# Optimization experiments

Measured on AMD Instinct MI355X. Metric: run time of the kernel, lower is better.

The kernel has to match this reference:

```python
import jax, jax.numpy as jnp
import numpy as np

N = 50000
E = 1600000
DIN = 100
D = 128
DOUT = 40
L = 3
EPS = 1e-5


def setup_inputs() -> dict:
    key = jax.random.key(0)
    ks = jax.random.split(key, 12)
    s = lambda *sh: 1.0 / np.sqrt(sh[-2] if len(sh) >= 2 else sh[-1])
    inp = {
        "x": jax.random.normal(ks[0], (N, DIN), jnp.float32),
        "edge_index": jax.random.randint(ks[1], (2, E), 0, N, jnp.int32),
        # node encoder (linear DIN -> D)
        "W_enc": jax.random.normal(ks[2], (DIN, D), jnp.float32) * (1.0 / np.sqrt(DIN)),
        "b_enc": jnp.zeros((D,), jnp.float32),
        # pre_mp linear D -> D
        "W_pre": jax.random.normal(ks[3], (D, D), jnp.float32) * (1.0 / np.sqrt(D)),
        "b_pre": jnp.zeros((D,), jnp.float32),
        # stacked GCN conv weights [L, D, D] and biases [L, D]
        "Wc": jax.random.normal(ks[4], (L, D, D), jnp.float32) * (1.0 / np.sqrt(D)),
        "bc": jnp.zeros((L, D), jnp.float32),
        # LayerNorm params for layers 0..L-2
        "ln_g": jnp.ones((L - 1, D), jnp.float32),
        "ln_b": jnp.zeros((L - 1, D), jnp.float32),
        # post_mp node head D -> DOUT
        "W_head": jax.random.normal(ks[5], (D, DOUT), jnp.float32) * (1.0 / np.sqrt(D)),
        "b_head": jnp.zeros((DOUT,), jnp.float32),
    }
    return inp


def _layer_norm(h, g, b):
    mu = jnp.mean(h, axis=-1, keepdims=True)
    var = jnp.mean(jnp.square(h - mu), axis=-1, keepdims=True)
    return (h - mu) * jax.lax.rsqrt(var + EPS) * g + b


def _gcn_forward(x, edge_index, W_enc, b_enc, W_pre, b_pre, Wc, bc, ln_g, ln_b, W_head, b_head):
    # feature encoder + pre-MP linear (dropout is identity in eval)
    h = x @ W_enc + b_enc
    h = h @ W_pre + b_pre

    # add self loops, compute symmetric GCN normalization once
    loop = jnp.arange(N, dtype=edge_index.dtype)
    src = jnp.concatenate([edge_index[0], loop])  # [E+N]
    dst = jnp.concatenate([edge_index[1], loop])
    deg = jax.ops.segment_sum(jnp.ones_like(dst, jnp.float32), dst, num_segments=N)
    dinv = jnp.where(deg > 0, jax.lax.rsqrt(jnp.maximum(deg, 1.0)), 0.0)
    norm = dinv[src] * dinv[dst]  # [E+N]

    for i in range(L):
        hw = h @ Wc[i]                              # [N, D] transform first
        msg = hw[src] * norm[:, None]               # gather + scale  [E+N, D]
        h = jax.ops.segment_sum(msg, dst, num_segments=N) + bc[i]
        if i < L - 1:
            h = _layer_norm(h, ln_g[i], ln_b[i])
            h = jax.nn.relu(h)
    # post-MP node classification head
    return h @ W_head + b_head


def reference(x, edge_index, W_enc, b_enc, W_pre, b_pre, Wc, bc, ln_g, ln_b, W_head, b_head):
    return _gcn_forward(x, edge_index, W_enc, b_enc, W_pre, b_pre, Wc, bc, ln_g, ln_b, W_head, b_head)
```

## Files before the change

kernel.cpp:

```cpp
#include <hip/hip_runtime.h>


#define NNODES 50000
#define NEDGES 1600000
#define DINN 100
#define DOUTN 40
#define CAP 96
#define NB1 ((NNODES + 255) / 256)
#define PDIV 687195u
#define NCHUNK 782
#define NGROUP 391
#define FE_GRID (NGROUP * 24)
#define MTILES ((NNODES + 63) / 64)

typedef __attribute__((ext_vector_type(8))) short short8;
typedef __attribute__((ext_vector_type(4))) float floatx4;

static __device__ __forceinline__ unsigned int f2bf(float f) {
    unsigned int u = __float_as_uint(f);
    return (u + 0x7fffu + ((u >> 16) & 1u)) >> 16;
}
static __device__ __forceinline__ float bflo(unsigned int u) { return __uint_as_float(u << 16); }
static __device__ __forceinline__ float bfhi(unsigned int u) { return __uint_as_float(u & 0xffff0000u); }

__global__ void init_ws(int* __restrict__ cursor, const float* __restrict__ Wpre,
                        const float* __restrict__ Wc, unsigned int* __restrict__ Wt) {
    int bid = blockIdx.x, tid = threadIdx.x;
    if (bid < NB1) {
        int n = bid * 256 + tid;
        if (n < NNODES) cursor[n] = 0;
    } else {
        int t = (bid - NB1) * 256 + tid;
        if (t < 4 * 8192) {
            int m = t >> 13, rem = t & 8191;
            int n = rem >> 6, k2 = rem & 63;
            const float* W = (m == 0) ? Wpre : (Wc + (size_t)(m - 1) * 16384);
            unsigned int lo = f2bf(W[(2 * k2) * 128 + n]);
            unsigned int hi = f2bf(W[(2 * k2 + 1) * 128 + n]);
            Wt[t] = lo | (hi << 16);
        }
    }
}

__global__ __launch_bounds__(256) void fill_enc(const int* __restrict__ src,
                                                const int* __restrict__ dst,
                                                int* __restrict__ cursor,
                                                unsigned short* __restrict__ colp,
                                                const float* __restrict__ x,
                                                const float* __restrict__ W_enc,
                                                const float* __restrict__ b_enc,
                                                unsigned int* __restrict__ C) {
    __shared__ float as[16][DINN];
    int bid = blockIdx.x, tid = threadIdx.x;
    int g = bid / 24, r = bid % 24;
    if (r < 16) {
        int p = bid & 7;
        int chunk = g * 2 + (r >> 3);
        int e0 = chunk * 2048;
#pragma unroll
        for (int k = 0; k < 8; k++) {
            int e = e0 + k * 256 + tid;
            if (e < NEDGES) {
                int d = dst[e];
                if ((int)(((unsigned long long)(unsigned)d * PDIV) >> 32) == p) {
                    int s = src[e];
                    int pos = atomicAdd(&cursor[d], 1);
                    if (pos < CAP) colp[(size_t)d * CAP + pos] = (unsigned short)s;
                }
            }
        }
    } else {
        int tile = g * 8 + (r - 16);
        int row0 = tile * 16;
        if (row0 >= NNODES) return;
        for (int idx = tid; idx < 16 * DINN; idx += 256) {
            int rr = idx / DINN, k = idx - rr * DINN;
            int row = row0 + rr;
            as[rr][k] = (row < NNODES) ? x[(size_t)row * DINN + k] : 0.0f;
        }
        __syncthreads();
        int c = tid & 63;
        int rg = tid >> 6;
        float acc0[4], acc1[4];
#pragma unroll
        for (int q = 0; q < 4; q++) { acc0[q] = 0.f; acc1[q] = 0.f; }
#pragma unroll 4
        for (int k = 0; k < DINN; k++) {
            float2 wv = *(const float2*)&W_enc[k * 128 + 2 * c];
#pragma unroll
            for (int q = 0; q < 4; q++) {
                float a = as[rg * 4 + q][k];
                acc0[q] += a * wv.x;
                acc1[q] += a * wv.y;
            }
        }
        float2 bb = *(const float2*)&b_enc[2 * c];
#pragma unroll
        for (int q = 0; q < 4; q++) {
            int row = row0 + rg * 4 + q;
            if (row < NNODES)
                C[(size_t)row * 64 + c] = f2bf(acc0[q] + bb.x) | (f2bf(acc1[q] + bb.y) << 16);
        }
    }
}

template <int MODE>
static __device__ __forceinline__ void mfma_body(unsigned char* smem, int bid,
                                                 const unsigned int* __restrict__ A,
                                                 const unsigned int* __restrict__ Bt,
                                                 const float* __restrict__ aux,
                                                 unsigned int* __restrict__ C, int M) {
    int tid = threadIdx.x;
    int row0 = bid * 64;
    for (int c = tid; c < 1024; c += 256) {
        int rr = c >> 4, c16 = c & 15;
        int grow = row0 + rr;
        uint4 p = (grow < M) ? *(const uint4*)&A[(size_t)grow * 64 + c16 * 4]
                             : make_uint4(0, 0, 0, 0);
        *(uint4*)&smem[(rr * 256 + c16 * 16) ^ ((rr & 7) << 4)] = p;
    }
    for (int c = tid; c < 2048; c += 256) {
        int n = c >> 4, k16 = c & 15;
        uint4 v = *(const uint4*)&Bt[n * 64 + k16 * 4];
        *(uint4*)&smem[16384 + ((n * 256 + k16 * 16) ^ ((n & 7) << 4))] = v;
    }
    __syncthreads();

    int lane = tid & 63, w = tid >> 6;
    int ml = lane & 15, kg = lane >> 4;
    short8 afrag[4];
#pragma unroll
    for (int k0 = 0; k0 < 4; k0++) {
        int rr = w * 16 + ml;
        uint4 t = *(uint4*)&smem[(rr * 256 + k0 * 64 + kg * 16) ^ ((rr & 7) << 4)];
        afrag[k0] = *(short8*)&t;
    }
#pragma unroll
    for (int n = 0; n < 8; n++) {
        floatx4 acc = {0.f, 0.f, 0.f, 0.f};
#pragma unroll
        for (int k0 = 0; k0 < 4; k0++) {
            int rn = n * 16 + ml;
            uint4 t = *(uint4*)&smem[16384 + ((rn * 256 + k0 * 64 + kg * 16) ^ ((rn & 7) << 4))];
            short8 b = *(short8*)&t;
            acc = __builtin_amdgcn_mfma_f32_16x16x32_bf16(afrag[k0], b, acc, 0, 0, 0);
        }
        int colc = n * 16 + ml;
        float bv = (MODE == 0) ? aux[colc] : 0.f;
#pragma unroll
        for (int q = 0; q < 4; q++) {
            int grow = row0 + w * 16 + kg * 4 + q;
            float v;
            if (MODE == 0) {
                v = acc[q] + bv;
            } else {
                float dv = (grow < M) ? aux[grow] : 0.f;
                v = acc[q] * dv;
            }
            float other = __shfl_xor(v, 1);
            if (!(lane & 1) && grow < M) {
                C[(size_t)grow * 64 + n * 8 + (ml >> 1)] = f2bf(v) | (f2bf(other) << 16);
            }
        }
    }
}

__global__ __launch_bounds__(256) void pre_mfma_dinv(const unsigned int* __restrict__ A,
                                                     const unsigned int* __restrict__ Bt,
                                                     const float* __restrict__ bias,
                                                     unsigned int* __restrict__ C,
                                                     const int* __restrict__ cursor,
                                                     float* __restrict__ dinv) {
    __shared__ __align__(16) unsigned char smem[49152];
    int bid = blockIdx.x;
    if (bid < MTILES) {
        mfma_body<0>(smem, bid, A, Bt, bias, C, NNODES);
    } else {
        int n = (bid - MTILES) * 256 + threadIdx.x;
        if (n < NNODES) dinv[n] = rsqrtf((float)(min(cursor[n], CAP) + 1));
    }
}

__global__ __launch_bounds__(256) void conv_mfma(const unsigned int* __restrict__ A,
                                                 const unsigned int* __restrict__ Bt,
                                                 const float* __restrict__ dinv,
                                                 unsigned int* __restrict__ C) {
    __shared__ __align__(16) unsigned char smem[49152];
    mfma_body<1>(smem, blockIdx.x, A, Bt, dinv, C, NNODES);
}

template <int LAST>
__global__ __launch_bounds__(256) void aggregate(const unsigned int* __restrict__ hw,
                                                 const unsigned short* __restrict__ colp,
                                                 const int* __restrict__ cursor,
                                                 const float* __restrict__ dinv,
                                                 const float* __restrict__ bias,
                                                 const float* __restrict__ g,
                                                 const float* __restrict__ b,
                                                 void* __restrict__ outv) {
    int row = blockIdx.x * 4 + (threadIdx.x >> 6);
    int lane = threadIdx.x & 63;
    if (row >= NNODES) return;
    int deg = min(cursor[row], CAP);
    const size_t cb = (size_t)row * CAP;
    unsigned int su = hw[(size_t)row * 64 + lane];
    float ax0 = bflo(su), ay0 = bfhi(su);
    float ax1 = 0.f, ay1 = 0.f, ax2 = 0.f, ay2 = 0.f, ax3 = 0.f, ay3 = 0.f;
    for (int j0 = 0; j0 < deg; j0 += 64) {
        int idx = j0 + lane;
        int myc = (idx < deg) ? (int)colp[cb + idx] : 0;
        int cnt = min(64, deg - j0);
        int j = 0;
        for (; j + 8 <= cnt; j += 8) {
            int s0 = __shfl(myc, j),     s1 = __shfl(myc, j + 1);
            int s2 = __shfl(myc, j + 2), s3 = __shfl(myc, j + 3);
            int s4 = __shfl(myc, j + 4), s5 = __shfl(myc, j + 5);
            int s6 = __shfl(myc, j + 6), s7 = __shfl(myc, j + 7);
            unsigned int u0 = hw[(size_t)s0 * 64 + lane];
            unsigned int u1 = hw[(size_t)s1 * 64 + lane];
            unsigned int u2 = hw[(size_t)s2 * 64 + lane];
            unsigned int u3 = hw[(size_t)s3 * 64 + lane];
            unsigned int u4 = hw[(size_t)s4 * 64 + lane];
            unsigned int u5 = hw[(size_t)s5 * 64 + lane];
            unsigned int u6 = hw[(size_t)s6 * 64 + lane];
            unsigned int u7 = hw[(size_t)s7 * 64 + lane];
            ax0 += bflo(u0); ay0 += bfhi(u0);
            ax1 += bflo(u1); ay1 += bfhi(u1);
            ax2 += bflo(u2); ay2 += bfhi(u2);
            ax3 += bflo(u3); ay3 += bfhi(u3);
            ax0 += bflo(u4); ay0 += bfhi(u4);
            ax1 += bflo(u5); ay1 += bfhi(u5);
            ax2 += bflo(u6); ay2 += bfhi(u6);
            ax3 += bflo(u7); ay3 += bfhi(u7);
        }
        for (; j < cnt; ++j) {
            int s = __shfl(myc, j);
            unsigned int u = hw[(size_t)s * 64 + lane];
            ax0 += bflo(u); ay0 += bfhi(u);
        }
    }
    float hx = ax0 + ax1 + ax2 + ax3;
    float hy = ay0 + ay1 + ay2 + ay3;
    float sc = dinv[row];
    float2 bb = *(const float2*)&bias[lane * 2];
    hx = hx * sc + bb.x;
    hy = hy * sc + bb.y;
    if (LAST == 0) {
        float sum = hx + hy;
#pragma unroll
        for (int off = 32; off >= 1; off >>= 1) sum += __shfl_xor(sum, off);
        float mu = sum * (1.0f / 128.0f);
        float dx = hx - mu, dy = hy - mu;
        float vs = dx * dx + dy * dy;
#pragma unroll
        for (int off = 32; off >= 1; off >>= 1) vs += __shfl_xor(vs, off);
        float rstd = rsqrtf(vs * (1.0f / 128.0f) + 1e-5f);
        float2 gg = *(const float2*)&g[lane * 2];
        float2 lb = *(const float2*)&b[lane * 2];
        hx = fmaxf(dx * rstd * gg.x + lb.x, 0.0f);
        hy = fmaxf(dy * rstd * gg.y + lb.y, 0.0f);
        ((unsigned int*)outv)[(size_t)row * 64 + lane] = f2bf(hx) | (f2bf(hy) << 16);
    } else {
        *(float2*)&((float*)outv)[(size_t)row * 128 + lane * 2] = make_float2(hx, hy);
    }
}

__global__ __launch_bounds__(256) void head_gemm(const float* __restrict__ h,
                                                 const float* __restrict__ W,
                                                 const float* __restrict__ bias,
                                                 float* __restrict__ out, int M) {
    __shared__ float hs[32][128];
    int tid = threadIdx.x;
    int row0 = blockIdx.x * 32;
    for (int idx = tid; idx < 32 * 128; idx += 256) {
        int rr = idx >> 7, k = idx & 127;
        int row = row0 + rr;
        hs[rr][k] = (row < M) ? h[(size_t)row * 128 + k] : 0.0f;
    }
    __syncthreads();
    int d = tid & 63;
    int rg = tid >> 6;
    if (d < DOUTN) {
        float acc[8];
#pragma unroll
        for (int q = 0; q < 8; q++) acc[q] = 0.0f;
#pragma unroll 4
        for (int k = 0; k < 128; k++) {
            float wv = W[k * DOUTN + d];
#pragma unroll
            for (int q = 0; q < 8; q++) acc[q] += hs[rg * 8 + q][k] * wv;
        }
        float bv = bias[d];
#pragma unroll
        for (int q = 0; q < 8; q++) {
            int row = row0 + rg * 8 + q;
            if (row < M) out[(size_t)row * DOUTN + d] = acc[q] + bv;
        }
    }
}

extern "C" void kernel_launch(void* const* d_in, const int* in_sizes, int n_in,
                              void* d_out, int out_size, void* d_ws, size_t ws_size,
                              hipStream_t stream) {
    const float* x = (const float*)d_in[0];
    const int* ei = (const int*)d_in[1];
    const int* esrc = ei;
    const int* edst = ei + NEDGES;
    const float* W_enc = (const float*)d_in[2];
    const float* b_enc = (const float*)d_in[3];
    const float* W_pre = (const float*)d_in[4];
    const float* b_pre = (const float*)d_in[5];
    const float* Wc = (const float*)d_in[6];
    const float* bc = (const float*)d_in[7];
    const float* ln_g = (const float*)d_in[8];
    const float* ln_b = (const float*)d_in[9];
    const float* W_head = (const float*)d_in[10];
    const float* b_head = (const float*)d_in[11];
    float* out = (float*)d_out;

    char* ws = (char*)d_ws;
    const size_t packBytes = (size_t)NNODES * 64 * 4;
    size_t off = 0;
    unsigned int* bufA = (unsigned int*)(ws + off); off += packBytes;
    unsigned int* bufB = (unsigned int*)(ws + off); off += packBytes;
    float* bufC = (float*)(ws + off); off += (size_t)NNODES * 128 * 4;
    float* dinv = (float*)(ws + off); off += (size_t)NNODES * 4;
    int* cursor = (int*)(ws + off); off += (size_t)NNODES * 4;
    unsigned int* Wt = (unsigned int*)(ws + off); off += (size_t)4 * 8192 * 4;
    unsigned short* colp = (unsigned short*)(ws + off); off += (size_t)NNODES * CAP * 2;

    init_ws<<<NB1 + 128, 256, 0, stream>>>(cursor, W_pre, Wc, Wt);

    fill_enc<<<FE_GRID, 256, 0, stream>>>(esrc, edst, cursor, colp, x, W_enc, b_enc, bufA);

    pre_mfma_dinv<<<MTILES + NB1, 256, 0, stream>>>(bufA, Wt, b_pre, bufB, cursor, dinv);

    for (int l = 0; l < 3; l++) {
        conv_mfma<<<MTILES, 256, 0, stream>>>(bufB, Wt + (size_t)(l + 1) * 8192, dinv, bufA);
        if (l < 2)
            aggregate<0><<<(NNODES + 3) / 4, 256, 0, stream>>>(
                bufA, colp, cursor, dinv, bc + (size_t)l * 128, ln_g + (size_t)l * 128,
                ln_b + (size_t)l * 128, bufB);
        else
            aggregate<1><<<(NNODES + 3) / 4, 256, 0, stream>>>(
                bufA, colp, cursor, dinv, bc + (size_t)l * 128, nullptr, nullptr, bufC);
    }

    head_gemm<<<(NNODES + 31) / 32, 256, 0, stream>>>(bufC, W_head, b_head, out, NNODES);
}
```

Baseline: 354.4 us.

## Fuse head GEMM into last aggregate and process two rows per wavefront

The aggregation kernel now handles two destination rows per wavefront and interleaves their neighbor gathers, so more independent loads are in flight. The final layer's aggregate computes the 128->40 head projection directly from registers with shuffles and a shared-memory copy of W_head. This removes the head_gemm kernel and the fp32 intermediate buffer round-trip. The dinv computation also drops the CAP clamp on degree, which changes the normalization when a node has more than CAP in-edges, and the shuffle-based head loop is serial per row.

```diff
diff --git a/kernel.cpp b/kernel.cpp
--- a/kernel.cpp
+++ b/kernel.cpp
@@ -8,7 +8,6 @@
 #define CAP 96
 #define NB1 ((NNODES + 255) / 256)
 #define PDIV 687195u
-#define NCHUNK 782
 #define NGROUP 391
 #define FE_GRID (NGROUP * 24)
 #define MTILES ((NNODES + 63) / 64)
@@ -177,7 +176,7 @@
         mfma_body<0>(smem, bid, A, Bt, bias, C, NNODES);
     } else {
         int n = (bid - MTILES) * 256 + threadIdx.x;
-        if (n < NNODES) dinv[n] = rsqrtf((float)(min(cursor[n], CAP) + 1));
+        if (n < NNODES) dinv[n] = rsqrtf((float)(cursor[n] + 1));
     }
 }
 
@@ -197,104 +196,122 @@
                                                  const float* __restrict__ bias,
                                                  const float* __restrict__ g,
                                                  const float* __restrict__ b,
-                                                 void* __restrict__ outv) {
-    int row = blockIdx.x * 4 + (threadIdx.x >> 6);
-    int lane = threadIdx.x & 63;
-    if (row >= NNODES) return;
-    int deg = min(cursor[row], CAP);
-    const size_t cb = (size_t)row * CAP;
-    unsigned int su = hw[(size_t)row * 64 + lane];
-    float ax0 = bflo(su), ay0 = bfhi(su);
-    float ax1 = 0.f, ay1 = 0.f, ax2 = 0.f, ay2 = 0.f, ax3 = 0.f, ay3 = 0.f;
-    for (int j0 = 0; j0 < deg; j0 += 64) {
-        int idx = j0 + lane;
-        int myc = (idx < deg) ? (int)colp[cb + idx] : 0;
-        int cnt = min(64, deg - j0);
-        int j = 0;
-        for (; j + 8 <= cnt; j += 8) {
-            int s0 = __shfl(myc, j),     s1 = __shfl(myc, j + 1);
-            int s2 = __shfl(myc, j + 2), s3 = __shfl(myc, j + 3);
-            int s4 = __shfl(myc, j + 4), s5 = __shfl(myc, j + 5);
-            int s6 = __shfl(myc, j + 6), s7 = __shfl(myc, j + 7);
-            unsigned int u0 = hw[(size_t)s0 * 64 + lane];
-            unsigned int u1 = hw[(size_t)s1 * 64 + lane];
-            unsigned int u2 = hw[(size_t)s2 * 64 + lane];
-            unsigned int u3 = hw[(size_t)s3 * 64 + lane];
-            unsigned int u4 = hw[(size_t)s4 * 64 + lane];
-            unsigned int u5 = hw[(size_t)s5 * 64 + lane];
-            unsigned int u6 = hw[(size_t)s6 * 64 + lane];
-            unsigned int u7 = hw[(size_t)s7 * 64 + lane];
-            ax0 += bflo(u0); ay0 += bfhi(u0);
-            ax1 += bflo(u1); ay1 += bfhi(u1);
-            ax2 += bflo(u2); ay2 += bfhi(u2);
-            ax3 += bflo(u3); ay3 += bfhi(u3);
-            ax0 += bflo(u4); ay0 += bfhi(u4);
-            ax1 += bflo(u5); ay1 += bfhi(u5);
-            ax2 += bflo(u6); ay2 += bfhi(u6);
-            ax3 += bflo(u7); ay3 += bfhi(u7);
-        }
-        for (; j < cnt; ++j) {
-            int s = __shfl(myc, j);
-            unsigned int u = hw[(size_t)s * 64 + lane];
+                                                 void* __restrict__ outv,
+                                                 const float* __restrict__ Wh,
+                                                 const float* __restrict__ bh) {
+    __shared__ float whs[LAST ? 128 * DOUTN : 1];
+    int tid = threadIdx.x, lane = tid & 63;
+    if (LAST) {
+        for (int i = tid; i < 128 * DOUTN; i += 256) whs[i] = Wh[i];
+        __syncthreads();
+    }
+    int wid = blockIdx.x * 4 + (tid >> 6);
+    int r0 = wid * 2;
+    if (r0 >= NNODES) return;
+    int r1 = r0 + 1;
+    int deg0 = min(cursor[r0], CAP), deg1 = min(cursor[r1], CAP);
+    const unsigned short* cp0 = &colp[(size_t)r0 * CAP];
+    const unsigned short* cp1 = &colp[(size_t)r1 * CAP];
+    int c0 = min(deg0, 64), c1 = min(deg1, 64);
+    int myc0 = (lane < c0) ? (int)cp0[lane] : 0;
+    int myc1 = (lane < c1) ? (int)cp1[lane] : 0;
+    float ax0 = 0.f, ay0 = 0.f, px0 = 0.f, py0 = 0.f;
+    float ax1 = 0.f, ay1 = 0.f, px1 = 0.f, py1 = 0.f;
+    int m = min(c0, c1) & ~7;
+    int j = 0;
+    for (; j < m; j += 8) {
+        int s0 = __shfl(myc0, j),     s1 = __shfl(myc0, j + 1);
+        int s2 = __shfl(myc0, j + 2), s3 = __shfl(myc0, j + 3);
+        int s4 = __shfl(myc0, j + 4), s5 = __shfl(myc0, j + 5);
+        int s6 = __shfl(myc0, j + 6), s7 = __shfl(myc0, j + 7);
+        int t0 = __shfl(myc1, j),     t1 = __shfl(myc1, j + 1);
+        int t2 = __shfl(myc1, j + 2), t3 = __shfl(myc1, j + 3);
+        int t4 = __shfl(myc1, j + 4), t5 = __shfl(myc1, j + 5);
+        int t6 = __shfl(myc1, j + 6), t7 = __shfl(myc1, j + 7);
+        unsigned u0 = hw[(size_t)s0 * 64 + lane], u1 = hw[(size_t)s1 * 64 + lane];
+        unsigned u2 = hw[(size_t)s2 * 64 + lane], u3 = hw[(size_t)s3 * 64 + lane];
+        unsigned u4 = hw[(size_t)s4 * 64 + lane], u5 = hw[(size_t)s5 * 64 + lane];
+        unsigned u6 = hw[(size_t)s6 * 64 + lane], u7 = hw[(size_t)s7 * 64 + lane];
+        unsigned v0 = hw[(size_t)t0 * 64 + lane], v1 = hw[(size_t)t1 * 64 + lane];
+        unsigned v2 = hw[(size_t)t2 * 64 + lane], v3 = hw[(size_t)t3 * 64 + lane];
+        unsigned v4 = hw[(size_t)t4 * 64 + lane], v5 = hw[(size_t)t5 * 64 + lane];
+        unsigned v6 = hw[(size_t)t6 * 64 + lane], v7 = hw[(size_t)t7 * 64 + lane];
+        ax0 += bflo(u0) + bflo(u1); ay0 += bfhi(u0) + bfhi(u1);
+        px0 += bflo(u2) + bflo(u3); py0 += bfhi(u2) + bfhi(u3);
+        ax0 += bflo(u4) + bflo(u5); ay0 += bfhi(u4) + bfhi(u5);
+        px0 += bflo(u6) + bflo(u7); py0 += bfhi(u6) + bfhi(u7);
+        ax1 += bflo(v0) + bflo(v1); ay1 += bfhi(v0) + bfhi(v1);
+        px1 += bflo(v2) + bflo(v3); py1 += bfhi(v2) + bfhi(v3);
+        ax1 += bflo(v4) + bflo(v5); ay1 += bfhi(v4) + bfhi(v5);
+        px1 += bflo(v6) + bflo(v7); py1 += bfhi(v6) + bfhi(v7);
+    }
+    for (; j < c0; ++j) {
+        int s = __shfl(myc0, j);
+        unsigned u = hw[(size_t)s * 64 + lane];
+        ax0 += bflo(u); ay0 += bfhi(u);
+    }
+    for (j = m; j < c1; ++j) {
+        int s = __shfl(myc1, j);
+        unsigned u = hw[(size_t)s * 64 + lane];
+        ax1 += bflo(u); ay1 += bfhi(u);
+    }
+    for (int j0 = 64; j0 < deg0; j0 += 64) {
+        int cc = min(64, deg0 - j0);
+        int mc = (lane < cc) ? (int)cp0[j0 + lane] : 0;
+        for (int k = 0; k < cc; ++k) {
+            int s = __shfl(mc, k);
+            unsigned u = hw[(size_t)s * 64 + lane];
             ax0 += bflo(u); ay0 += bfhi(u);
         }
     }
-    float hx = ax0 + ax1 + ax2 + ax3;
-    float hy = ay0 + ay1 + ay2 + ay3;
-    float sc = dinv[row];
-    float2 bb = *(const float2*)&bias[lane * 2];
-    hx = hx * sc + bb.x;
-    hy = hy * sc + bb.y;
-    if (LAST == 0) {
-        float sum = hx + hy;
-#pragma unroll
-        for (int off = 32; off >= 1; off >>= 1) sum += __shfl_xor(sum, off);
-        float mu = sum * (1.0f / 128.0f);
-        float dx = hx - mu, dy = hy - mu;
-        float vs = dx * dx + dy * dy;
-#pragma unroll
-        for (int off = 32; off >= 1; off >>= 1) vs += __shfl_xor(vs, off);
-        float rstd = rsqrtf(vs * (1.0f / 128.0f) + 1e-5f);
-        float2 gg = *(const float2*)&g[lane * 2];
-        float2 lb = *(const float2*)&b[lane * 2];
-        hx = fmaxf(dx * rstd * gg.x + lb.x, 0.0f);
-        hy = fmaxf(dy * rstd * gg.y + lb.y, 0.0f);
-        ((unsigned int*)outv)[(size_t)row * 64 + lane] = f2bf(hx) | (f2bf(hy) << 16);
-    } else {
-        *(float2*)&((float*)outv)[(size_t)row * 128 + lane * 2] = make_float2(hx, hy);
-    }
-}
-
-__global__ __launch_bounds__(256) void head_gemm(const float* __restrict__ h,
-                                                 const float* __restrict__ W,
-                                                 const float* __restrict__ bias,
-                                                 float* __restrict__ out, int M) {
-    __shared__ float hs[32][128];
-    int tid = threadIdx.x;
-    int row0 = blockIdx.x * 32;
-    for (int idx = tid; idx < 32 * 128; idx += 256) {
-        int rr = idx >> 7, k = idx & 127;
-        int row = row0 + rr;
-        hs[rr][k] = (row < M) ? h[(size_t)row * 128 + k] : 0.0f;
-    }
-    __syncthreads();
-    int d = tid & 63;
-    int rg = tid >> 6;
-    if (d < DOUTN) {
-        float acc[8];
-#pragma unroll
-        for (int q = 0; q < 8; q++) acc[q] = 0.0f;
+    for (int j0 = 64; j0 < deg1; j0 += 64) {
+        int cc = min(64, deg1 - j0);
+        int mc = (lane < cc) ? (int)cp1[j0 + lane] : 0;
+        for (int k = 0; k < cc; ++k) {
+            int s = __shfl(mc, k);
+            unsigned u = hw[(size_t)s * 64 + lane];
+            ax1 += bflo(u); ay1 += bfhi(u);
+        }
+    }
+
+    float hxa[2] = {ax0 + px0, ax1 + px1};
+    float hya[2] = {ay0 + py0, ay1 + py1};
+#pragma unroll
+    for (int q = 0; q < 2; q++) {
+        int row = r0 + q;
+        unsigned su = hw[(size_t)row * 64 + lane];
+        float hx = hxa[q] + bflo(su);
+        float hy = hya[q] + bfhi(su);
+        float sc = dinv[row];
+        float2 bb = *(const float2*)&bias[lane * 2];
+        hx = hx * sc + bb.x;
+        hy = hy * sc + bb.y;
+        if (LAST == 0) {
+            float sum = hx + hy;
+#pragma unroll
+            for (int off = 32; off >= 1; off >>= 1) sum += __shfl_xor(sum, off);
+            float mu = sum * (1.0f / 128.0f);
+            float dx = hx - mu, dy = hy - mu;
+            float vs = dx * dx + dy * dy;
+#pragma unroll
+            for (int off = 32; off >= 1; off >>= 1) vs += __shfl_xor(vs, off);
+            float rstd = rsqrtf(vs * (1.0f / 128.0f) + 1e-5f);
+            float2 gg = *(const float2*)&g[lane * 2];
+            float2 lb = *(const float2*)&b[lane * 2];
+            hx = fmaxf(dx * rstd * gg.x + lb.x, 0.0f);
+            hy = fmaxf(dy * rstd * gg.y + lb.y, 0.0f);
+            ((unsigned int*)outv)[(size_t)row * 64 + lane] = f2bf(hx) | (f2bf(hy) << 16);
+        } else {
+            float acc = (lane < DOUTN) ? bh[lane] : 0.f;
 #pragma unroll 4
-        for (int k = 0; k < 128; k++) {
-            float wv = W[k * DOUTN + d];
-#pragma unroll
-            for (int q = 0; q < 8; q++) acc[q] += hs[rg * 8 + q][k] * wv;
-        }
-        float bv = bias[d];
-#pragma unroll
-        for (int q = 0; q < 8; q++) {
-            int row = row0 + rg * 8 + q;
-            if (row < M) out[(size_t)row * DOUTN + d] = acc[q] + bv;
+            for (int k = 0; k < 64; k++) {
+                float hxk = __shfl(hx, k);
+                float hyk = __shfl(hy, k);
+                if (lane < DOUTN)
+                    acc += hxk * whs[(2 * k) * DOUTN + lane] +
+                           hyk * whs[(2 * k + 1) * DOUTN + lane];
+            }
+            if (lane < DOUTN) ((float*)outv)[(size_t)row * DOUTN + lane] = acc;
         }
     }
 }
@@ -323,7 +340,6 @@
     size_t off = 0;
     unsigned int* bufA = (unsigned int*)(ws + off); off += packBytes;
     unsigned int* bufB = (unsigned int*)(ws + off); off += packBytes;
-    float* bufC = (float*)(ws + off); off += (size_t)NNODES * 128 * 4;
     float* dinv = (float*)(ws + off); off += (size_t)NNODES * 4;
     int* cursor = (int*)(ws + off); off += (size_t)NNODES * 4;
     unsigned int* Wt = (unsigned int*)(ws + off); off += (size_t)4 * 8192 * 4;
@@ -338,13 +354,12 @@
     for (int l = 0; l < 3; l++) {
         conv_mfma<<<MTILES, 256, 0, stream>>>(bufB, Wt + (size_t)(l + 1) * 8192, dinv, bufA);
         if (l < 2)
-            aggregate<0><<<(NNODES + 3) / 4, 256, 0, stream>>>(
+            aggregate<0><<<(NNODES / 8), 256, 0, stream>>>(
                 bufA, colp, cursor, dinv, bc + (size_t)l * 128, ln_g + (size_t)l * 128,
-                ln_b + (size_t)l * 128, bufB);
+                ln_b + (size_t)l * 128, bufB, nullptr, nullptr);
         else
-            aggregate<1><<<(NNODES + 3) / 4, 256, 0, stream>>>(
-                bufA, colp, cursor, dinv, bc + (size_t)l * 128, nullptr, nullptr, bufC);
-    }
-
-    head_gemm<<<(NNODES + 31) / 32, 256, 0, stream>>>(bufC, W_head, b_head, out, NNODES);
-}
+            aggregate<1><<<(NNODES / 8), 256, 0, stream>>>(
+                bufA, colp, cursor, dinv, bc + (size_t)l * 128, nullptr, nullptr, out,
+                W_head, b_head);
+    }
+}
```

Result: slower. 419.0 us (+18.2%).

## Split GCN aggregation into two feature-half passes for cache-resident gathers

Applied to the files above, without the earlier changes.

The conv GEMM now writes its output as two separate 64-column bf16 halves. Aggregation runs as two kernels, one per half, so each gather table is 6.4 MB instead of 12.8 MB and is more likely to stay in cache; each wavefront processes two edges at once with half-width rows. The first half's fp32 result is staged in a scratch buffer, and the second kernel reads it back to apply LayerNorm. This costs an extra launch and extra scratch traffic. The dinv computation also changes to use the uncapped degree.

```diff
diff --git a/kernel.cpp b/kernel.cpp
--- a/kernel.cpp
+++ b/kernel.cpp
@@ -8,7 +8,6 @@
 #define CAP 96
 #define NB1 ((NNODES + 255) / 256)
 #define PDIV 687195u
-#define NCHUNK 782
 #define NGROUP 391
 #define FE_GRID (NGROUP * 24)
 #define MTILES ((NNODES + 63) / 64)
@@ -109,7 +108,8 @@
                                                  const unsigned int* __restrict__ A,
                                                  const unsigned int* __restrict__ Bt,
                                                  const float* __restrict__ aux,
-                                                 unsigned int* __restrict__ C, int M) {
+                                                 unsigned int* __restrict__ C,
+                                                 unsigned int* __restrict__ CB, int M) {
     int tid = threadIdx.x;
     int row0 = bid * 64;
     for (int c = tid; c < 1024; c += 256) {
@@ -159,7 +159,15 @@
             }
             float other = __shfl_xor(v, 1);
             if (!(lane & 1) && grow < M) {
-                C[(size_t)grow * 64 + n * 8 + (ml >> 1)] = f2bf(v) | (f2bf(other) << 16);
+                unsigned int pk = f2bf(v) | (f2bf(other) << 16);
+                if (MODE == 0) {
+                    C[(size_t)grow * 64 + n * 8 + (ml >> 1)] = pk;
+                } else {
+                    if (n < 4)
+                        C[(size_t)grow * 32 + n * 8 + (ml >> 1)] = pk;
+                    else
+                        CB[(size_t)grow * 32 + (n - 4) * 8 + (ml >> 1)] = pk;
+                }
             }
         }
     }
@@ -174,94 +182,128 @@
     __shared__ __align__(16) unsigned char smem[49152];
     int bid = blockIdx.x;
     if (bid < MTILES) {
-        mfma_body<0>(smem, bid, A, Bt, bias, C, NNODES);
+        mfma_body<0>(smem, bid, A, Bt, bias, C, nullptr, NNODES);
     } else {
         int n = (bid - MTILES) * 256 + threadIdx.x;
-        if (n < NNODES) dinv[n] = rsqrtf((float)(min(cursor[n], CAP) + 1));
+        if (n < NNODES) dinv[n] = rsqrtf((float)(cursor[n] + 1));
     }
 }
 
 __global__ __launch_bounds__(256) void conv_mfma(const unsigned int* __restrict__ A,
                                                  const unsigned int* __restrict__ Bt,
                                                  const float* __restrict__ dinv,
-                                                 unsigned int* __restrict__ C) {
+                                                 unsigned int* __restrict__ CA,
+                                                 unsigned int* __restrict__ CB) {
     __shared__ __align__(16) unsigned char smem[49152];
-    mfma_body<1>(smem, blockIdx.x, A, Bt, dinv, C, NNODES);
-}
-
-template <int LAST>
-__global__ __launch_bounds__(256) void aggregate(const unsigned int* __restrict__ hw,
-                                                 const unsigned short* __restrict__ colp,
-                                                 const int* __restrict__ cursor,
-                                                 const float* __restrict__ dinv,
-                                                 const float* __restrict__ bias,
-                                                 const float* __restrict__ g,
-                                                 const float* __restrict__ b,
-                                                 void* __restrict__ outv) {
-    int row = blockIdx.x * 4 + (threadIdx.x >> 6);
-    int lane = threadIdx.x & 63;
+    mfma_body<1>(smem, blockIdx.x, A, Bt, dinv, CA, CB, NNODES);
+}
+
+template <int H, int LAST>
+__global__ __launch_bounds__(256) void aggregate_half(const unsigned int* __restrict__ hw,
+                                                      const unsigned short* __restrict__ colp,
+                                                      const int* __restrict__ cursor,
+                                                      const float* __restrict__ dinv,
+                                                      const float* __restrict__ bias,
+                                                      const float* __restrict__ g,
+                                                      const float* __restrict__ b,
+                                                      float* __restrict__ sA,
+                                                      void* __restrict__ outv) {
+    int tid = threadIdx.x, lane = tid & 63;
+    int row = blockIdx.x * 4 + (tid >> 6);
     if (row >= NNODES) return;
+    int lh = lane & 31;
+    int hi = lane >> 5;
     int deg = min(cursor[row], CAP);
-    const size_t cb = (size_t)row * CAP;
-    unsigned int su = hw[(size_t)row * 64 + lane];
-    float ax0 = bflo(su), ay0 = bfhi(su);
-    float ax1 = 0.f, ay1 = 0.f, ax2 = 0.f, ay2 = 0.f, ax3 = 0.f, ay3 = 0.f;
-    for (int j0 = 0; j0 < deg; j0 += 64) {
-        int idx = j0 + lane;
-        int myc = (idx < deg) ? (int)colp[cb + idx] : 0;
-        int cnt = min(64, deg - j0);
-        int j = 0;
-        for (; j + 8 <= cnt; j += 8) {
-            int s0 = __shfl(myc, j),     s1 = __shfl(myc, j + 1);
-            int s2 = __shfl(myc, j + 2), s3 = __shfl(myc, j + 3);
-            int s4 = __shfl(myc, j + 4), s5 = __shfl(myc, j + 5);
-            int s6 = __shfl(myc, j + 6), s7 = __shfl(myc, j + 7);
-            unsigned int u0 = hw[(size_t)s0 * 64 + lane];
-            unsigned int u1 = hw[(size_t)s1 * 64 + lane];
-            unsigned int u2 = hw[(size_t)s2 * 64 + lane];
-            unsigned int u3 = hw[(size_t)s3 * 64 + lane];
-            unsigned int u4 = hw[(size_t)s4 * 64 + lane];
-            unsigned int u5 = hw[(size_t)s5 * 64 + lane];
-            unsigned int u6 = hw[(size_t)s6 * 64 + lane];
-            unsigned int u7 = hw[(size_t)s7 * 64 + lane];
-            ax0 += bflo(u0); ay0 += bfhi(u0);
-            ax1 += bflo(u1); ay1 += bfhi(u1);
-            ax2 += bflo(u2); ay2 += bfhi(u2);
-            ax3 += bflo(u3); ay3 += bfhi(u3);
-            ax0 += bflo(u4); ay0 += bfhi(u4);
-            ax1 += bflo(u5); ay1 += bfhi(u5);
-            ax2 += bflo(u6); ay2 += bfhi(u6);
-            ax3 += bflo(u7); ay3 += bfhi(u7);
-        }
-        for (; j < cnt; ++j) {
-            int s = __shfl(myc, j);
-            unsigned int u = hw[(size_t)s * 64 + lane];
-            ax0 += bflo(u); ay0 += bfhi(u);
-        }
-    }
-    float hx = ax0 + ax1 + ax2 + ax3;
-    float hy = ay0 + ay1 + ay2 + ay3;
+    const unsigned short* cp = &colp[(size_t)row * CAP];
+    int cnt = min(deg, 64);
+    int myc = (lane < cnt) ? (int)cp[lane] : 0;
+    float ax = 0.f, ay = 0.f, px = 0.f, py = 0.f;
+    int j0 = 0;
+    for (; j0 + 16 <= cnt; j0 += 16) {
+        int e = j0 + hi;
+        int s0 = __shfl(myc, e),      s1 = __shfl(myc, e + 2);
+        int s2 = __shfl(myc, e + 4),  s3 = __shfl(myc, e + 6);
+        int s4 = __shfl(myc, e + 8),  s5 = __shfl(myc, e + 10);
+        int s6 = __shfl(myc, e + 12), s7 = __shfl(myc, e + 14);
+        unsigned u0 = hw[(size_t)s0 * 32 + lh], u1 = hw[(size_t)s1 * 32 + lh];
+        unsigned u2 = hw[(size_t)s2 * 32 + lh], u3 = hw[(size_t)s3 * 32 + lh];
+        unsigned u4 = hw[(size_t)s4 * 32 + lh], u5 = hw[(size_t)s5 * 32 + lh];
+        unsigned u6 = hw[(size_t)s6 * 32 + lh], u7 = hw[(size_t)s7 * 32 + lh];
+        ax += bflo(u0) + bflo(u1); ay += bfhi(u0) + bfhi(u1);
+        px += bflo(u2) + bflo(u3); py += bfhi(u2) + bfhi(u3);
+        ax += bflo(u4) + bflo(u5); ay += bfhi(u4) + bfhi(u5);
+        px += bflo(u6) + bflo(u7); py += bfhi(u6) + bfhi(u7);
+    }
+    if (j0 < cnt) {
+        int e = j0 + hi;
+        int cm = cnt - 1;
+        int s0 = __shfl(myc, min(e, cm)),      s1 = __shfl(myc, min(e + 2, cm));
+        int s2 = __shfl(myc, min(e + 4, cm)),  s3 = __shfl(myc, min(e + 6, cm));
+        int s4 = __shfl(myc, min(e + 8, cm)),  s5 = __shfl(myc, min(e + 10, cm));
+        int s6 = __shfl(myc, min(e + 12, cm)), s7 = __shfl(myc, min(e + 14, cm));
+        unsigned u0 = (e < cnt) ? hw[(size_t)s0 * 32 + lh] : 0u;
+        unsigned u1 = (e + 2 < cnt) ? hw[(size_t)s1 * 32 + lh] : 0u;
+        unsigned u2 = (e + 4 < cnt) ? hw[(size_t)s2 * 32 + lh] : 0u;
+        unsigned u3 = (e + 6 < cnt) ? hw[(size_t)s3 * 32 + lh] : 0u;
+        unsigned u4 = (e + 8 < cnt) ? hw[(size_t)s4 * 32 + lh] : 0u;
+        unsigned u5 = (e + 10 < cnt) ? hw[(size_t)s5 * 32 + lh] : 0u;
+        unsigned u6 = (e + 12 < cnt) ? hw[(size_t)s6 * 32 + lh] : 0u;
+        unsigned u7 = (e + 14 < cnt) ? hw[(size_t)s7 * 32 + lh] : 0u;
+        ax += bflo(u0) + bflo(u1); ay += bfhi(u0) + bfhi(u1);
+        px += bflo(u2) + bflo(u3); py += bfhi(u2) + bfhi(u3);
+        ax += bflo(u4) + bflo(u5); ay += bfhi(u4) + bfhi(u5);
+        px += bflo(u6) + bflo(u7); py += bfhi(u6) + bfhi(u7);
+    }
+    for (int base = 64; base < deg; base += 64) {
+        int cc = min(64, deg - base);
+        int mc = (lane < cc) ? (int)cp[base + lane] : 0;
+        for (int j = 0; j < cc; j += 2) {
+            int e = j + hi;
+            int s = __shfl(mc, min(e, cc - 1));
+            unsigned u = (e < cc) ? hw[(size_t)s * 32 + lh] : 0u;
+            ax += bflo(u); ay += bfhi(u);
+        }
+    }
+    ax += px; ay += py;
+    ax += __shfl_xor(ax, 32);
+    ay += __shfl_xor(ay, 32);
+    unsigned su = hw[(size_t)row * 32 + lh];
     float sc = dinv[row];
-    float2 bb = *(const float2*)&bias[lane * 2];
-    hx = hx * sc + bb.x;
-    hy = hy * sc + bb.y;
-    if (LAST == 0) {
-        float sum = hx + hy;
-#pragma unroll
-        for (int off = 32; off >= 1; off >>= 1) sum += __shfl_xor(sum, off);
-        float mu = sum * (1.0f / 128.0f);
-        float dx = hx - mu, dy = hy - mu;
-        float vs = dx * dx + dy * dy;
-#pragma unroll
-        for (int off = 32; off >= 1; off >>= 1) vs += __shfl_xor(vs, off);
-        float rstd = rsqrtf(vs * (1.0f / 128.0f) + 1e-5f);
-        float2 gg = *(const float2*)&g[lane * 2];
-        float2 lb = *(const float2*)&b[lane * 2];
-        hx = fmaxf(dx * rstd * gg.x + lb.x, 0.0f);
-        hy = fmaxf(dy * rstd * gg.y + lb.y, 0.0f);
-        ((unsigned int*)outv)[(size_t)row * 64 + lane] = f2bf(hx) | (f2bf(hy) << 16);
+    float2 bb = *(const float2*)&bias[(H ? 64 : 0) + 2 * lh];
+    float hx = (ax + bflo(su)) * sc + bb.x;
+    float hy = (ay + bfhi(su)) * sc + bb.y;
+    if (H == 0) {
+        if (LAST == 0) {
+            if (hi == 0) *(float2*)&sA[(size_t)row * 64 + 2 * lh] = make_float2(hx, hy);
+        } else {
+            if (hi == 0)
+                *(float2*)&((float*)outv)[(size_t)row * 128 + 2 * lh] = make_float2(hx, hy);
+        }
     } else {
-        *(float2*)&((float*)outv)[(size_t)row * 128 + lane * 2] = make_float2(hx, hy);
+        if (LAST == 1) {
+            if (hi == 1)
+                *(float2*)&((float*)outv)[(size_t)row * 128 + 64 + 2 * lh] =
+                    make_float2(hx, hy);
+        } else {
+            float2 av = *(const float2*)&sA[(size_t)row * 64 + 2 * lh];
+            float sum = av.x + av.y + hx + hy;
+#pragma unroll
+            for (int off = 16; off >= 1; off >>= 1) sum += __shfl_xor(sum, off);
+            float mu = sum * (1.0f / 128.0f);
+            float dA0 = av.x - mu, dA1 = av.y - mu;
+            float dB0 = hx - mu, dB1 = hy - mu;
+            float vs = dA0 * dA0 + dA1 * dA1 + dB0 * dB0 + dB1 * dB1;
+#pragma unroll
+            for (int off = 16; off >= 1; off >>= 1) vs += __shfl_xor(vs, off);
+            float rstd = rsqrtf(vs * (1.0f / 128.0f) + 1e-5f);
+            float v0 = hi ? dB0 : dA0;
+            float v1 = hi ? dB1 : dA1;
+            float2 gg = *(const float2*)&g[2 * lane];
+            float2 lb = *(const float2*)&b[2 * lane];
+            float o0 = fmaxf(v0 * rstd * gg.x + lb.x, 0.0f);
+            float o1 = fmaxf(v1 * rstd * gg.y + lb.y, 0.0f);
+            ((unsigned int*)outv)[(size_t)row * 64 + lane] = f2bf(o0) | (f2bf(o1) << 16);
+        }
     }
 }
 
@@ -319,10 +361,12 @@
     float* out = (float*)d_out;
 
     char* ws = (char*)d_ws;
-    const size_t packBytes = (size_t)NNODES * 64 * 4;
     size_t off = 0;
-    unsigned int* bufA = (unsigned int*)(ws + off); off += packBytes;
-    unsigned int* bufB = (unsigned int*)(ws + off); off += packBytes;
+    unsigned int* F1 = (unsigned int*)(ws + off); off += (size_t)NNODES * 64 * 4;
+    unsigned int* F2 = (unsigned int*)(ws + off); off += (size_t)NNODES * 64 * 4;
+    unsigned int* hwA = (unsigned int*)(ws + off); off += (size_t)NNODES * 32 * 4;
+    unsigned int* hwB = (unsigned int*)(ws + off); off += (size_t)NNODES * 32 * 4;
+    float* sA = (float*)(ws + off); off += (size_t)NNODES * 64 * 4;
     float* bufC = (float*)(ws + off); off += (size_t)NNODES * 128 * 4;
     float* dinv = (float*)(ws + off); off += (size_t)NNODES * 4;
     int* cursor = (int*)(ws + off); off += (size_t)NNODES * 4;
@@ -331,19 +375,25 @@
 
     init_ws<<<NB1 + 128, 256, 0, stream>>>(cursor, W_pre, Wc, Wt);
 
-    fill_enc<<<FE_GRID, 256, 0, stream>>>(esrc, edst, cursor, colp, x, W_enc, b_enc, bufA);
-
-    pre_mfma_dinv<<<MTILES + NB1, 256, 0, stream>>>(bufA, Wt, b_pre, bufB, cursor, dinv);
-
+    fill_enc<<<FE_GRID, 256, 0, stream>>>(esrc, edst, cursor, colp, x, W_enc, b_enc, F1);
+
+    pre_mfma_dinv<<<MTILES + NB1, 256, 0, stream>>>(F1, Wt, b_pre, F2, cursor, dinv);
+
+    const int AGG_GRID = (NNODES + 3) / 4;
     for (int l = 0; l < 3; l++) {
-        conv_mfma<<<MTILES, 256, 0, stream>>>(bufB, Wt + (size_t)(l + 1) * 8192, dinv, bufA);
-        if (l < 2)
-            aggregate<0><<<(NNODES + 3) / 4, 256, 0, stream>>>(
-                bufA, colp, cursor, dinv, bc + (size_t)l * 128, ln_g + (size_t)l * 128,
-                ln_b + (size_t)l * 128, bufB);
-        else
-            aggregate<1><<<(NNODES + 3) / 4, 256, 0, stream>>>(
-                bufA, colp, cursor, dinv, bc + (size_t)l * 128, nullptr, nullptr, bufC);
+        conv_mfma<<<MTILES, 256, 0, stream>>>(F2, Wt + (size_t)(l + 1) * 8192, dinv, hwA, hwB);
+        if (l < 2) {
+            aggregate_half<0, 0><<<AGG_GRID, 256, 0, stream>>>(
+                hwA, colp, cursor, dinv, bc + (size_t)l * 128, nullptr, nullptr, sA, F2);
+            aggregate_half<1, 0><<<AGG_GRID, 256, 0, stream>>>(
+                hwB, colp, cursor, dinv, bc + (size_t)l * 128, ln_g + (size_t)l * 128,
+                ln_b + (size_t)l * 128, sA, F2);
+        } else {
+            aggregate_half<0, 1><<<AGG_GRID, 256, 0, stream>>>(
+                hwA, colp, cursor, dinv, bc + (size_t)l * 128, nullptr, nullptr, sA, bufC);
+            aggregate_half<1, 1><<<AGG_GRID, 256, 0, stream>>>(
+                hwB, colp, cursor, dinv, bc + (size_t)l * 128, nullptr, nullptr, sA, bufC);
+        }
     }
 
     head_gemm<<<(NNODES + 31) / 32, 256, 0, stream>>>(bufC, W_head, b_head, out, NNODES);
```

After: 364.2 us. 1.03x slower.

## Fold pre-MP linear into first conv weight and compute dinv inline

Applied to the files above, without the earlier changes.

Precomputes W_pre·Wc[0] and b_pre·Wc[0] in the init kernel, so the separate pre-MP GEMM pass over all nodes is removed and the first conv GEMM adds the folded bias before degree scaling. The dinv array is dropped; both the conv GEMM epilogue and the aggregation recompute rsqrt(deg+1) from the cursor counts. The final aggregation now writes bf16 packed features instead of fp32, which halves the traffic into the head GEMM. The trade-offs are bf16 rounding of the fused weight product and final activations. The normalisation now uses the uncapped degree, which differs from the earlier capped value whenever a node exceeds CAP.

```diff
diff --git a/kernel.cpp b/kernel.cpp
--- a/kernel.cpp
+++ b/kernel.cpp
@@ -8,7 +8,6 @@
 #define CAP 96
 #define NB1 ((NNODES + 255) / 256)
 #define PDIV 687195u
-#define NCHUNK 782
 #define NGROUP 391
 #define FE_GRID (NGROUP * 24)
 #define MTILES ((NNODES + 63) / 64)
@@ -24,20 +23,40 @@
 static __device__ __forceinline__ float bfhi(unsigned int u) { return __uint_as_float(u & 0xffff0000u); }
 
 __global__ void init_ws(int* __restrict__ cursor, const float* __restrict__ Wpre,
-                        const float* __restrict__ Wc, unsigned int* __restrict__ Wt) {
+                        const float* __restrict__ Wc, const float* __restrict__ b_pre,
+                        unsigned int* __restrict__ Wt, float* __restrict__ v0) {
     int bid = blockIdx.x, tid = threadIdx.x;
     if (bid < NB1) {
         int n = bid * 256 + tid;
         if (n < NNODES) cursor[n] = 0;
+    } else if (bid < NB1 + 64) {
+        int tt = (bid - NB1) * 256 + tid;
+        int mm = 2 + (tt >> 13);
+        int rem = tt & 8191;
+        int n = rem >> 6, k2 = rem & 63;
+        const float* W = Wc + (size_t)(mm - 1) * 16384;
+        unsigned int lo = f2bf(W[(2 * k2) * 128 + n]);
+        unsigned int hi = f2bf(W[(2 * k2 + 1) * 128 + n]);
+        Wt[mm * 8192 + n * 64 + k2] = lo | (hi << 16);
+    } else if (bid < NB1 + 96) {
+        int t = (bid - NB1 - 64) * 256 + tid;
+        int n = t >> 6, k2 = t & 63;
+        const float* wp0 = Wpre + (size_t)(2 * k2) * 128;
+        const float* wp1 = wp0 + 128;
+        float d0 = 0.f, d1 = 0.f;
+#pragma unroll 4
+        for (int j = 0; j < 128; j++) {
+            float wc = Wc[j * 128 + n];
+            d0 += wp0[j] * wc;
+            d1 += wp1[j] * wc;
+        }
+        Wt[8192 + n * 64 + k2] = f2bf(d0) | (f2bf(d1) << 16);
     } else {
-        int t = (bid - NB1) * 256 + tid;
-        if (t < 4 * 8192) {
-            int m = t >> 13, rem = t & 8191;
-            int n = rem >> 6, k2 = rem & 63;
-            const float* W = (m == 0) ? Wpre : (Wc + (size_t)(m - 1) * 16384);
-            unsigned int lo = f2bf(W[(2 * k2) * 128 + n]);
-            unsigned int hi = f2bf(W[(2 * k2 + 1) * 128 + n]);
-            Wt[t] = lo | (hi << 16);
+        if (tid < 128) {
+            float d = 0.f;
+#pragma unroll 4
+            for (int j = 0; j < 128; j++) d += b_pre[j] * Wc[j * 128 + tid];
+            v0[tid] = d;
         }
     }
 }
@@ -104,14 +123,16 @@
     }
 }
 
-template <int MODE>
-static __device__ __forceinline__ void mfma_body(unsigned char* smem, int bid,
-                                                 const unsigned int* __restrict__ A,
+template <int BIASV>
+__global__ __launch_bounds__(256) void conv_mfma(const unsigned int* __restrict__ A,
                                                  const unsigned int* __restrict__ Bt,
-                                                 const float* __restrict__ aux,
-                                                 unsigned int* __restrict__ C, int M) {
+                                                 const int* __restrict__ cursor,
+                                                 const float* __restrict__ v0,
+                                                 unsigned int* __restrict__ C) {
+    __shared__ __align__(16) unsigned char smem[49152];
     int tid = threadIdx.x;
-    int row0 = bid * 64;
+    int row0 = blockIdx.x * 64;
+    const int M = NNODES;
     for (int c = tid; c < 1024; c += 256) {
         int rr = c >> 4, c16 = c & 15;
         int grow = row0 + rr;
@@ -135,6 +156,12 @@
         uint4 t = *(uint4*)&smem[(rr * 256 + k0 * 64 + kg * 16) ^ ((rr & 7) << 4)];
         afrag[k0] = *(short8*)&t;
     }
+    float dvq[4];
+#pragma unroll
+    for (int q = 0; q < 4; q++) {
+        int grow = row0 + w * 16 + kg * 4 + q;
+        dvq[q] = (grow < M) ? rsqrtf((float)(cursor[grow] + 1)) : 0.f;
+    }
 #pragma unroll
     for (int n = 0; n < 8; n++) {
         floatx4 acc = {0.f, 0.f, 0.f, 0.f};
@@ -146,17 +173,11 @@
             acc = __builtin_amdgcn_mfma_f32_16x16x32_bf16(afrag[k0], b, acc, 0, 0, 0);
         }
         int colc = n * 16 + ml;
-        float bv = (MODE == 0) ? aux[colc] : 0.f;
+        float bv = BIASV ? v0[colc] : 0.f;
 #pragma unroll
         for (int q = 0; q < 4; q++) {
             int grow = row0 + w * 16 + kg * 4 + q;
-            float v;
-            if (MODE == 0) {
-                v = acc[q] + bv;
-            } else {
-                float dv = (grow < M) ? aux[grow] : 0.f;
-                v = acc[q] * dv;
-            }
+            float v = (acc[q] + bv) * dvq[q];
             float other = __shfl_xor(v, 1);
             if (!(lane & 1) && grow < M) {
                 C[(size_t)grow * 64 + n * 8 + (ml >> 1)] = f2bf(v) | (f2bf(other) << 16);
@@ -165,50 +186,26 @@
     }
 }
 
-__global__ __launch_bounds__(256) void pre_mfma_dinv(const unsigned int* __restrict__ A,
-                                                     const unsigned int* __restrict__ Bt,
-                                                     const float* __restrict__ bias,
-                                                     unsigned int* __restrict__ C,
-                                                     const int* __restrict__ cursor,
-                                                     float* __restrict__ dinv) {
-    __shared__ __align__(16) unsigned char smem[49152];
-    int bid = blockIdx.x;
-    if (bid < MTILES) {
-        mfma_body<0>(smem, bid, A, Bt, bias, C, NNODES);
-    } else {
-        int n = (bid - MTILES) * 256 + threadIdx.x;
-        if (n < NNODES) dinv[n] = rsqrtf((float)(min(cursor[n], CAP) + 1));
-    }
-}
-
-__global__ __launch_bounds__(256) void conv_mfma(const unsigned int* __restrict__ A,
-                                                 const unsigned int* __restrict__ Bt,
-                                                 const float* __restrict__ dinv,
-                                                 unsigned int* __restrict__ C) {
-    __shared__ __align__(16) unsigned char smem[49152];
-    mfma_body<1>(smem, blockIdx.x, A, Bt, dinv, C, NNODES);
-}
-
 template <int LAST>
 __global__ __launch_bounds__(256) void aggregate(const unsigned int* __restrict__ hw,
                                                  const unsigned short* __restrict__ colp,
                                                  const int* __restrict__ cursor,
-                                                 const float* __restrict__ dinv,
                                                  const float* __restrict__ bias,
                                                  const float* __restrict__ g,
                                                  const float* __restrict__ b,
-                                                 void* __restrict__ outv) {
+                                                 unsigned int* __restrict__ outp) {
     int row = blockIdx.x * 4 + (threadIdx.x >> 6);
     int lane = threadIdx.x & 63;
     if (row >= NNODES) return;
-    int deg = min(cursor[row], CAP);
-    const size_t cb = (size_t)row * CAP;
+    int curs = cursor[row];
+    int deg = min(curs, CAP);
+    const unsigned short* cp = &colp[(size_t)row * CAP];
     unsigned int su = hw[(size_t)row * 64 + lane];
     float ax0 = bflo(su), ay0 = bfhi(su);
     float ax1 = 0.f, ay1 = 0.f, ax2 = 0.f, ay2 = 0.f, ax3 = 0.f, ay3 = 0.f;
     for (int j0 = 0; j0 < deg; j0 += 64) {
         int idx = j0 + lane;
-        int myc = (idx < deg) ? (int)colp[cb + idx] : 0;
+        int myc = (idx < deg) ? (int)cp[idx] : 0;
         int cnt = min(64, deg - j0);
         int j = 0;
         for (; j + 8 <= cnt; j += 8) {
@@ -216,14 +213,14 @@
             int s2 = __shfl(myc, j + 2), s3 = __shfl(myc, j + 3);
             int s4 = __shfl(myc, j + 4), s5 = __shfl(myc, j + 5);
             int s6 = __shfl(myc, j + 6), s7 = __shfl(myc, j + 7);
-            unsigned int u0 = hw[(size_t)s0 * 64 + lane];
-            unsigned int u1 = hw[(size_t)s1 * 64 + lane];
-            unsigned int u2 = hw[(size_t)s2 * 64 + lane];
-            unsigned int u3 = hw[(size_t)s3 * 64 + lane];
-            unsigned int u4 = hw[(size_t)s4 * 64 + lane];
-            unsigned int u5 = hw[(size_t)s5 * 64 + lane];
-            unsigned int u6 = hw[(size_t)s6 * 64 + lane];
-            unsigned int u7 = hw[(size_t)s7 * 64 + lane];
+            unsigned u0 = hw[(size_t)s0 * 64 + lane];
+            unsigned u1 = hw[(size_t)s1 * 64 + lane];
+            unsigned u2 = hw[(size_t)s2 * 64 + lane];
+            unsigned u3 = hw[(size_t)s3 * 64 + lane];
+            unsigned u4 = hw[(size_t)s4 * 64 + lane];
+            unsigned u5 = hw[(size_t)s5 * 64 + lane];
+            unsigned u6 = hw[(size_t)s6 * 64 + lane];
+            unsigned u7 = hw[(size_t)s7 * 64 + lane];
             ax0 += bflo(u0); ay0 += bfhi(u0);
             ax1 += bflo(u1); ay1 += bfhi(u1);
             ax2 += bflo(u2); ay2 += bfhi(u2);
@@ -235,13 +232,13 @@
         }
         for (; j < cnt; ++j) {
             int s = __shfl(myc, j);
-            unsigned int u = hw[(size_t)s * 64 + lane];
+            unsigned u = hw[(size_t)s * 64 + lane];
             ax0 += bflo(u); ay0 += bfhi(u);
         }
     }
     float hx = ax0 + ax1 + ax2 + ax3;
     float hy = ay0 + ay1 + ay2 + ay3;
-    float sc = dinv[row];
+    float sc = rsqrtf((float)(curs + 1));
     float2 bb = *(const float2*)&bias[lane * 2];
     hx = hx * sc + bb.x;
     hy = hy * sc + bb.y;
@@ -259,23 +256,23 @@
         float2 lb = *(const float2*)&b[lane * 2];
         hx = fmaxf(dx * rstd * gg.x + lb.x, 0.0f);
         hy = fmaxf(dy * rstd * gg.y + lb.y, 0.0f);
-        ((unsigned int*)outv)[(size_t)row * 64 + lane] = f2bf(hx) | (f2bf(hy) << 16);
-    } else {
-        *(float2*)&((float*)outv)[(size_t)row * 128 + lane * 2] = make_float2(hx, hy);
-    }
-}
-
-__global__ __launch_bounds__(256) void head_gemm(const float* __restrict__ h,
+    }
+    outp[(size_t)row * 64 + lane] = f2bf(hx) | (f2bf(hy) << 16);
+}
+
+__global__ __launch_bounds__(256) void head_gemm(const unsigned int* __restrict__ h,
                                                  const float* __restrict__ W,
                                                  const float* __restrict__ bias,
                                                  float* __restrict__ out, int M) {
     __shared__ float hs[32][128];
     int tid = threadIdx.x;
     int row0 = blockIdx.x * 32;
-    for (int idx = tid; idx < 32 * 128; idx += 256) {
-        int rr = idx >> 7, k = idx & 127;
+    for (int idx = tid; idx < 32 * 64; idx += 256) {
+        int rr = idx >> 6, c = idx & 63;
         int row = row0 + rr;
-        hs[rr][k] = (row < M) ? h[(size_t)row * 128 + k] : 0.0f;
+        unsigned u = (row < M) ? h[(size_t)row * 64 + c] : 0u;
+        hs[rr][2 * c] = bflo(u);
+        hs[rr][2 * c + 1] = bfhi(u);
     }
     __syncthreads();
     int d = tid & 63;
@@ -321,30 +318,28 @@
     char* ws = (char*)d_ws;
     const size_t packBytes = (size_t)NNODES * 64 * 4;
     size_t off = 0;
-    unsigned int* bufA = (unsigned int*)(ws + off); off += packBytes;
-    unsigned int* bufB = (unsigned int*)(ws + off); off += packBytes;
-    float* bufC = (float*)(ws + off); off += (size_t)NNODES * 128 * 4;
-    float* dinv = (float*)(ws + off); off += (size_t)NNODES * 4;
+    unsigned int* F1 = (unsigned int*)(ws + off); off += packBytes;
+    unsigned int* F2 = (unsigned int*)(ws + off); off += packBytes;
+    unsigned int* hw = (unsigned int*)(ws + off); off += packBytes;
     int* cursor = (int*)(ws + off); off += (size_t)NNODES * 4;
     unsigned int* Wt = (unsigned int*)(ws + off); off += (size_t)4 * 8192 * 4;
+    float* v0 = (float*)(ws + off); off += 512;
     unsigned short* colp = (unsigned short*)(ws + off); off += (size_t)NNODES * CAP * 2;
 
-    init_ws<<<NB1 + 128, 256, 0, stream>>>(cursor, W_pre, Wc, Wt);
-
-    fill_enc<<<FE_GRID, 256, 0, stream>>>(esrc, edst, cursor, colp, x, W_enc, b_enc, bufA);
-
-    pre_mfma_dinv<<<MTILES + NB1, 256, 0, stream>>>(bufA, Wt, b_pre, bufB, cursor, dinv);
-
-    for (int l = 0; l < 3; l++) {
-        conv_mfma<<<MTILES, 256, 0, stream>>>(bufB, Wt + (size_t)(l + 1) * 8192, dinv, bufA);
-        if (l < 2)
-            aggregate<0><<<(NNODES + 3) / 4, 256, 0, stream>>>(
-                bufA, colp, cursor, dinv, bc + (size_t)l * 128, ln_g + (size_t)l * 128,
-                ln_b + (size_t)l * 128, bufB);
-        else
-            aggregate<1><<<(NNODES + 3) / 4, 256, 0, stream>>>(
-                bufA, colp, cursor, dinv, bc + (size_t)l * 128, nullptr, nullptr, bufC);
-    }
-
-    head_gemm<<<(NNODES + 31) / 32, 256, 0, stream>>>(bufC, W_head, b_head, out, NNODES);
-}
+    init_ws<<<NB1 + 97, 256, 0, stream>>>(cursor, W_pre, Wc, b_pre, Wt, v0);
+
+    fill_enc<<<FE_GRID, 256, 0, stream>>>(esrc, edst, cursor, colp, x, W_enc, b_enc, F1);
+
+    conv_mfma<1><<<MTILES, 256, 0, stream>>>(F1, Wt + 8192, cursor, v0, hw);
+    aggregate<0><<<(NNODES + 3) / 4, 256, 0, stream>>>(hw, colp, cursor, bc, ln_g, ln_b, F2);
+
+    conv_mfma<0><<<MTILES, 256, 0, stream>>>(F2, Wt + 2 * 8192, cursor, nullptr, hw);
+    aggregate<0><<<(NNODES + 3) / 4, 256, 0, stream>>>(hw, colp, cursor, bc + 128, ln_g + 128,
+                                                       ln_b + 128, F2);
+
+    conv_mfma<0><<<MTILES, 256, 0, stream>>>(F2, Wt + 3 * 8192, cursor, nullptr, hw);
+    aggregate<1><<<(NNODES + 3) / 4, 256, 0, stream>>>(hw, colp, cursor, bc + 256, nullptr,
+                                                       nullptr, F2);
+
+    head_gemm<<<(NNODES + 31) / 32, 256, 0, stream>>>(F2, W_head, b_head, out, NNODES);
+}
```

Result: faster. 326.1 us, median of 2 (-8.0%).
